# Optimization experiments

Hardware: AMD Instinct MI355X
Metric: run time of the kernel (lower is better)

## Reference

```python
import jax, jax.numpy as jnp
import numpy as np

N_NODES = 100000
N_EDGES = 1600000
D_IN = 64
D_OUT = 64
ALPHA = 0.5


def setup_inputs() -> dict:
    key = jax.random.key(0)
    k_x, k_ei, k_w, k_ws, k_bs, k_wd, k_bd = jax.random.split(key, 7)
    x = jax.random.normal(k_x, (N_NODES, D_IN), dtype=jnp.float32)
    edge_index = jax.random.randint(k_ei, (2, N_EDGES), 0, N_NODES, dtype=jnp.int64)
    edge_weight = jax.random.uniform(k_w, (N_EDGES,), dtype=jnp.float32)
    # torch Linear init: uniform(-1/sqrt(fan_in), 1/sqrt(fan_in))
    bound = 1.0 / np.sqrt(D_IN)
    W_src = jax.random.uniform(k_ws, (D_OUT, D_IN), minval=-bound, maxval=bound, dtype=jnp.float32)
    b_src = jax.random.uniform(k_bs, (D_OUT,), minval=-bound, maxval=bound, dtype=jnp.float32)
    W_dst = jax.random.uniform(k_wd, (D_OUT, D_IN), minval=-bound, maxval=bound, dtype=jnp.float32)
    b_dst = jax.random.uniform(k_bd, (D_OUT,), minval=-bound, maxval=bound, dtype=jnp.float32)
    return {"x": x, "edge_index": edge_index, "edge_weight": edge_weight,
            "W_src": W_src, "b_src": b_src, "W_dst": W_dst, "b_dst": b_dst}


def _dir_norm_spmm(row, col, w, x, n):
    """Compute (D_out^{-1/2} A D_in^{-1/2}) @ x for A with entries (row, col, w)."""
    out_deg = jax.ops.segment_sum(w, row, num_segments=n)  # row sums (dim=1)
    in_deg = jax.ops.segment_sum(w, col, num_segments=n)   # col sums (dim=0)
    d_out = jnp.where(out_deg > 0, out_deg ** -0.5, 0.0)
    d_in = jnp.where(in_deg > 0, in_deg ** -0.5, 0.0)
    w_norm = w * d_out[row] * d_in[col]                    # [E]
    # SpMM: out[i] = sum_{e: row_e = i} w_norm_e * x[col_e]
    return jax.ops.segment_sum(w_norm[:, None] * x[col], row, num_segments=n)


def reference(x, edge_index, edge_weight, W_src, b_src, W_dst, b_dst):
    row, col = edge_index[0], edge_index[1]
    n = x.shape[0]
    agg_fwd = _dir_norm_spmm(row, col, edge_weight, x, n)   # adj_norm @ x
    agg_bwd = _dir_norm_spmm(col, row, edge_weight, x, n)   # adj_t_norm @ x
    out = ALPHA * (agg_fwd @ W_src.T + b_src) + (1.0 - ALPHA) * (agg_bwd @ W_dst.T + b_dst)
    return out
```

## Files before the change

### kernel.cpp

```cpp
#include <hip/hip_runtime.h>

#define D 64
#define ALPHA 0.5f
#define FXSCALE 16777216.f
#define CE 2048
#define BSH 9
#define BN 512

typedef unsigned long long u64;
typedef unsigned short u16;
typedef unsigned int u32;
typedef float f32x4 __attribute__((ext_vector_type(4)));

static __device__ __forceinline__ u16 f2bf(float f) {
    unsigned u = __float_as_uint(f);
    unsigned r = (u + 0x7fffu + ((u >> 16) & 1u)) >> 16;
    return (u16)r;
}
static __device__ __forceinline__ float bf2f(u16 h) {
    return __uint_as_float(((unsigned)h) << 16);
}
static __device__ __forceinline__ float dinv_of_fx(u32 fx) {
    float s = (float)fx * (1.f / FXSCALE);
    return (s > 0.f) ? rsqrtf(s) : 0.f;
}

__global__ void p1_hist_kernel(const int* __restrict__ row, const int* __restrict__ col,
                               int* __restrict__ bh, int N, int E, int NCH, int NBUCK) {
    __shared__ u32 h[512];
    int t = threadIdx.x, ch = blockIdx.x;
    h[t] = 0;
    __syncthreads();
    int e0 = ch * CE, e1 = min(E, e0 + CE);
    for (int e = e0 + t; e < e1; e += 512) {
        atomicAdd(&h[(u32)row[e] >> BSH], 1u);
        atomicAdd(&h[(u32)(N + col[e]) >> BSH], 1u);
    }
    __syncthreads();
    for (int b = t; b < NBUCK; b += 512)
        bh[(size_t)b * NCH + ch] = (int)h[b];
}

__global__ void scan1i_kernel(const int* __restrict__ src, int* __restrict__ bsum, int SZ) {
    __shared__ int s[512];
    int t = threadIdx.x;
    int i = blockIdx.x * 512 + t;
    s[t] = (i < SZ) ? src[i] : 0;
    __syncthreads();
    for (int off = 256; off; off >>= 1) {
        if (t < off) s[t] += s[t + off];
        __syncthreads();
    }
    if (t == 0) bsum[blockIdx.x] = s[0];
}

__global__ void scan2w_kernel(int* __restrict__ bsum, int nb) {
    __shared__ int s[1024];
    int t = threadIdx.x;
    int v = (t < nb) ? bsum[t] : 0;
    s[t] = v;
    __syncthreads();
    for (int off = 1; off < 1024; off <<= 1) {
        int u = (t >= off) ? s[t - off] : 0;
        __syncthreads();
        s[t] += u;
        __syncthreads();
    }
    if (t < nb) bsum[t] = s[t] - v;
}

__global__ void scan3i_kernel(const int* __restrict__ src, const int* __restrict__ bsum,
                              int* __restrict__ dst, int SZ) {
    __shared__ int s[512];
    int t = threadIdx.x;
    int i = blockIdx.x * 512 + t;
    int v = (i < SZ) ? src[i] : 0;
    s[t] = v;
    __syncthreads();
    for (int off = 1; off < 512; off <<= 1) {
        int u = (t >= off) ? s[t - off] : 0;
        __syncthreads();
        s[t] += u;
        __syncthreads();
    }
    if (i < SZ) dst[i] = bsum[blockIdx.x] + s[t] - v;
}

__global__ void p3_sort_kernel(const int* __restrict__ row, const int* __restrict__ col,
                               const float* __restrict__ w,
                               const int* __restrict__ scanned,
                               u64* __restrict__ ent, int N, int E, int NCH, int NBUCK) {
    __shared__ u64 ebuf[4096];
    __shared__ u16 ebkt[4096];
    __shared__ u32 hc[512], hstart[512], hoff[512];
    __shared__ int s[512];
    int t = threadIdx.x, ch = blockIdx.x;
    hc[t] = 0;
    __syncthreads();
    int e0 = ch * CE, e1 = min(E, e0 + CE);
    for (int e = e0 + t; e < e1; e += 512) {
        atomicAdd(&hc[(u32)row[e] >> BSH], 1u);
        atomicAdd(&hc[(u32)(N + col[e]) >> BSH], 1u);
    }
    __syncthreads();
    int v = (int)hc[t];
    s[t] = v;
    __syncthreads();
    for (int off = 1; off < 512; off <<= 1) {
        int u = (t >= off) ? s[t - off] : 0;
        __syncthreads();
        s[t] += u;
        __syncthreads();
    }
    hstart[t] = (u32)(s[t] - v);
    hoff[t]   = (u32)(s[t] - v);
    hc[t] = (t < NBUCK) ? (u32)scanned[(size_t)t * NCH + ch] : 0u;
    __syncthreads();
    for (int e = e0 + t; e < e1; e += 512) {
        int r = row[e], c = col[e];
        u32 wb = __float_as_uint(w[e]);
        u32 b1 = (u32)r >> BSH;
        u64 q1 = ((u64)wb << 32) | ((u32)c << BSH) | ((u32)r & (BN - 1));
        u32 p1 = atomicAdd(&hoff[b1], 1u);
        ebuf[p1] = q1; ebkt[p1] = (u16)b1;
        u32 d2 = (u32)(N + c);
        u32 b2 = d2 >> BSH;
        u64 q2 = ((u64)wb << 32) | ((u32)r << BSH) | (d2 & (BN - 1));
        u32 p2 = atomicAdd(&hoff[b2], 1u);
        ebuf[p2] = q2; ebkt[p2] = (u16)b2;
    }
    __syncthreads();
    int nent = 2 * (e1 - e0);
    for (int p = t; p < nent; p += 512) {
        u32 b = ebkt[p];
        ent[(size_t)hc[b] + (u32)p - hstart[b]] = ebuf[p];
    }
}

__global__ void p4_build_kernel(const u64* __restrict__ ent, const int* __restrict__ scanned,
                                float* __restrict__ dinv, int* __restrict__ ptr,
                                float2* __restrict__ edata,
                                int L, int NCH, int NBUCK, int total) {
    __shared__ u32 cnt[512], fx[512], pstart[512], pfill[512];
    __shared__ int s[512];
    int t = threadIdx.x, b = blockIdx.x;
    int base0 = scanned[(size_t)b * NCH];
    int base1 = (b + 1 < NBUCK) ? scanned[(size_t)(b + 1) * NCH] : total;
    int nE = base1 - base0;
    cnt[t] = 0; fx[t] = 0;
    __syncthreads();
    for (int i = t; i < nE; i += 512) {
        u64 q = ent[base0 + i];
        u32 dlo = (u32)q & (BN - 1);
        float wv = __uint_as_float((u32)(q >> 32));
        atomicAdd(&cnt[dlo], 1u);
        atomicAdd(&fx[dlo], (u32)__float2uint_rn(wv * FXSCALE));
    }
    __syncthreads();
    int v = (int)cnt[t];
    s[t] = v;
    __syncthreads();
    for (int off = 1; off < 512; off <<= 1) {
        int u = (t >= off) ? s[t - off] : 0;
        __syncthreads();
        s[t] += u;
        __syncthreads();
    }
    pstart[t] = (u32)(s[t] - v);
    pfill[t]  = (u32)(s[t] - v);
    int node = b * BN + t;
    if (node < L) {
        dinv[node] = dinv_of_fx(fx[t]);
        ptr[node] = base0 + (int)pstart[t];
    }
    if (b == 0 && t == 0) ptr[L] = total;
    __syncthreads();
    for (int i = t; i < nE; i += 512) {
        u64 q = ent[base0 + i];
        u32 dlo = (u32)q & (BN - 1);
        u32 src = ((u32)q) >> BSH;
        float wv = __uint_as_float((u32)(q >> 32));
        u32 pos = atomicAdd(&pfill[dlo], 1u);
        edata[base0 + pos] = make_float2(__int_as_float((int)src), wv);
    }
}

__global__ void transform2r_kernel(const float* __restrict__ x,
                                   const float* __restrict__ Ws, const float* __restrict__ Wd,
                                   const float* __restrict__ dinv,
                                   u16* __restrict__ y1, u16* __restrict__ y2, int N) {
    __shared__ float xs[64][65];
    __shared__ float Wt1[64][68];
    __shared__ float Wt2[64][68];
    int t = threadIdx.x;
    for (int i = t; i < 4096; i += 256) {
        int o = i >> 6, k = i & 63;
        Wt1[k][o] = Ws[i];
        Wt2[k][o] = Wd[i];
    }
    int r0 = blockIdx.x * 64;
    for (int i = t; i < 4096; i += 256) {
        int r = i >> 6, k = i & 63;
        int gr = r0 + r;
        xs[r][k] = (gr < N) ? x[(size_t)gr * D + k] : 0.f;
    }
    __syncthreads();
    int ro = t >> 4, co = t & 15;
    float a1[4][4] = {}, a2[4][4] = {};
#pragma unroll 4
    for (int k = 0; k < 64; ++k) {
        float v0 = xs[ro * 4 + 0][k];
        float v1 = xs[ro * 4 + 1][k];
        float v2 = xs[ro * 4 + 2][k];
        float v3 = xs[ro * 4 + 3][k];
        float4 b1 = *(const float4*)&Wt1[k][co * 4];
        float4 b2 = *(const float4*)&Wt2[k][co * 4];
        a1[0][0] += v0 * b1.x; a1[0][1] += v0 * b1.y; a1[0][2] += v0 * b1.z; a1[0][3] += v0 * b1.w;
        a1[1][0] += v1 * b1.x; a1[1][1] += v1 * b1.y; a1[1][2] += v1 * b1.z; a1[1][3] += v1 * b1.w;
        a1[2][0] += v2 * b1.x; a1[2][1] += v2 * b1.y; a1[2][2] += v2 * b1.z; a1[2][3] += v2 * b1.w;
        a1[3][0] += v3 * b1.x; a1[3][1] += v3 * b1.y; a1[3][2] += v3 * b1.z; a1[3][3] += v3 * b1.w;
        a2[0][0] += v0 * b2.x; a2[0][1] += v0 * b2.y; a2[0][2] += v0 * b2.z; a2[0][3] += v0 * b2.w;
        a2[1][0] += v1 * b2.x; a2[1][1] += v1 * b2.y; a2[1][2] += v1 * b2.z; a2[1][3] += v1 * b2.w;
        a2[2][0] += v2 * b2.x; a2[2][1] += v2 * b2.y; a2[2][2] += v2 * b2.z; a2[2][3] += v2 * b2.w;
        a2[3][0] += v3 * b2.x; a2[3][1] += v3 * b2.y; a2[3][2] += v3 * b2.z; a2[3][3] += v3 * b2.w;
    }
#pragma unroll
    for (int i = 0; i < 4; ++i) {
        int gr = r0 + ro * 4 + i;
        if (gr < N) {
            float d1 = ALPHA * dinv[N + gr];
            float d2 = (1.f - ALPHA) * dinv[gr];
            ushort4 o1, o2;
            o1.x = f2bf(a1[i][0] * d1); o1.y = f2bf(a1[i][1] * d1);
            o1.z = f2bf(a1[i][2] * d1); o1.w = f2bf(a1[i][3] * d1);
            o2.x = f2bf(a2[i][0] * d2); o2.y = f2bf(a2[i][1] * d2);
            o2.z = f2bf(a2[i][2] * d2); o2.w = f2bf(a2[i][3] * d2);
            *(ushort4*)&y1[(size_t)gr * D + co * 4] = o1;
            *(ushort4*)&y2[(size_t)gr * D + co * 4] = o2;
        }
    }
}

__global__ void gather_csr_kernel(const int* __restrict__ ptr, const float* __restrict__ dinv,
                                  const float2* __restrict__ ed,
                                  const u16* __restrict__ y1, const u16* __restrict__ y2,
                                  const float* __restrict__ b_src, const float* __restrict__ b_dst,
                                  float* __restrict__ out, int N) {
    int tid = threadIdx.x;
    int lane = tid & 63;
    int node = blockIdx.x * (blockDim.x >> 6) + (tid >> 6);
    if (node >= N) return;
    int g  = lane >> 4;
    int fl = lane & 15;
    float dout = dinv[node], din = dinv[N + node];

    float f0 = 0.f, f1 = 0.f, f2 = 0.f, f3 = 0.f;
    float b0 = 0.f, b1 = 0.f, b2 = 0.f, b3 = 0.f;

    {
        int e0 = ptr[node], e1 = ptr[node + 1];
        for (int eb = e0; eb < e1; eb += 8) {
            int ea = eb + g, ex = eb + 4 + g;
            float2 da = (ea < e1) ? ed[ea] : make_float2(__int_as_float(0), 0.f);
            float2 db = (ex < e1) ? ed[ex] : make_float2(__int_as_float(0), 0.f);
            int sa = __float_as_int(da.x), sb = __float_as_int(db.x);
            float wa = da.y, wb = db.y;
            u64 qa = *(const u64*)(y1 + (((size_t)sa) << 6) + (fl << 2));
            u64 qb = *(const u64*)(y1 + (((size_t)sb) << 6) + (fl << 2));
            f0 += wa * bf2f((u16)qa)         + wb * bf2f((u16)qb);
            f1 += wa * bf2f((u16)(qa >> 16)) + wb * bf2f((u16)(qb >> 16));
            f2 += wa * bf2f((u16)(qa >> 32)) + wb * bf2f((u16)(qb >> 32));
            f3 += wa * bf2f((u16)(qa >> 48)) + wb * bf2f((u16)(qb >> 48));
        }
    }
    {
        int e0 = ptr[N + node], e1 = ptr[N + node + 1];
        for (int eb = e0; eb < e1; eb += 8) {
            int ea = eb + g, ex = eb + 4 + g;
            float2 da = (ea < e1) ? ed[ea] : make_float2(__int_as_float(0), 0.f);
            float2 db = (ex < e1) ? ed[ex] : make_float2(__int_as_float(0), 0.f);
            int sa = __float_as_int(da.x), sb = __float_as_int(db.x);
            float wa = da.y, wb = db.y;
            u64 qa = *(const u64*)(y2 + (((size_t)sa) << 6) + (fl << 2));
            u64 qb = *(const u64*)(y2 + (((size_t)sb) << 6) + (fl << 2));
            b0 += wa * bf2f((u16)qa)         + wb * bf2f((u16)qb);
            b1 += wa * bf2f((u16)(qa >> 16)) + wb * bf2f((u16)(qb >> 16));
            b2 += wa * bf2f((u16)(qa >> 32)) + wb * bf2f((u16)(qb >> 32));
            b3 += wa * bf2f((u16)(qa >> 48)) + wb * bf2f((u16)(qb >> 48));
        }
    }
    float v0 = f0 * dout + b0 * din;
    float v1 = f1 * dout + b1 * din;
    float v2 = f2 * dout + b2 * din;
    float v3 = f3 * dout + b3 * din;
    v0 += __shfl_xor(v0, 16); v0 += __shfl_xor(v0, 32);
    v1 += __shfl_xor(v1, 16); v1 += __shfl_xor(v1, 32);
    v2 += __shfl_xor(v2, 16); v2 += __shfl_xor(v2, 32);
    v3 += __shfl_xor(v3, 16); v3 += __shfl_xor(v3, 32);
    if (g == 0) {
        float4 bs = *(const float4*)&b_src[fl << 2];
        float4 bd = *(const float4*)&b_dst[fl << 2];
        f32x4 o;
        o.x = v0 + ALPHA * bs.x + (1.f - ALPHA) * bd.x;
        o.y = v1 + ALPHA * bs.y + (1.f - ALPHA) * bd.y;
        o.z = v2 + ALPHA * bs.z + (1.f - ALPHA) * bd.z;
        o.w = v3 + ALPHA * bs.w + (1.f - ALPHA) * bd.w;
        __builtin_nontemporal_store(o, (f32x4*)&out[((size_t)node << 6) + (fl << 2)]);
    }
}

extern "C" void kernel_launch(void* const* d_in, const int* in_sizes, int n_in,
                              void* d_out, int out_size, void* d_ws, size_t ws_size,
                              hipStream_t stream) {
    const float* x     = (const float*)d_in[0];
    const int*   ei    = (const int*)d_in[1];
    const float* w     = (const float*)d_in[2];
    const float* W_src = (const float*)d_in[3];
    const float* b_src = (const float*)d_in[4];
    const float* W_dst = (const float*)d_in[5];
    const float* b_dst = (const float*)d_in[6];
    float* out = (float*)d_out;

    const int N = in_sizes[0] / D;
    const int E = in_sizes[2];
    const int* row = ei;
    const int* col = ei + E;
    const int L = 2 * N;
    const int NCH   = (E + CE - 1) / CE;
    const int NBUCK = (L + BN - 1) >> BSH;
    const int SZ    = NBUCK * NCH;
    const int NSB   = (SZ + 511) / 512;
    const int total = 2 * E;

    char* base = (char*)d_ws;
    size_t o = 0;
    auto take = [&](size_t b) { char* p = base + o; o = (o + b + 63) & ~(size_t)63; return p; };
    int*    bh      = (int*)take((size_t)SZ * 4);
    int*    scanned = (int*)take((size_t)SZ * 4);
    int*    bsum    = (int*)take(1024 * 4);
    u64*    ent     = (u64*)take((size_t)total * 8);
    float*  dinv    = (float*)take((size_t)L * 4);
    int*    ptr     = (int*)take((size_t)(L + 1) * 4);
    u16*    y1      = (u16*)take((size_t)N * D * 2);
    u16*    y2      = (u16*)take((size_t)N * D * 2);
    float2* edata   = (float2*)take((size_t)total * 8);

    p1_hist_kernel<<<NCH, 512, 0, stream>>>(row, col, bh, N, E, NCH, NBUCK);
    scan1i_kernel<<<NSB, 512, 0, stream>>>(bh, bsum, SZ);
    scan2w_kernel<<<1, 1024, 0, stream>>>(bsum, NSB);
    scan3i_kernel<<<NSB, 512, 0, stream>>>(bh, bsum, scanned, SZ);
    p3_sort_kernel<<<NCH, 512, 0, stream>>>(row, col, w, scanned, ent, N, E, NCH, NBUCK);
    p4_build_kernel<<<NBUCK, 512, 0, stream>>>(ent, scanned, dinv, ptr, edata,
                                               L, NCH, NBUCK, total);
    transform2r_kernel<<<(N + 63) / 64, 256, 0, stream>>>(x, W_src, W_dst, dinv, y1, y2, N);
    gather_csr_kernel<<<(N + 3) / 4, 256, 0, stream>>>(ptr, dinv, edata, y1, y2,
                                                       b_src, b_dst, out, N);
}
```

Baseline: 233.7 us.

## Fuse dense transform into sort kernel and move source-degree scaling into gather

After: 217.1 us. 1.08x faster.

```diff
diff --git a/kernel.cpp b/kernel.cpp
--- a/kernel.cpp
+++ b/kernel.cpp
@@ -86,54 +86,111 @@
     if (i < SZ) dst[i] = bsum[blockIdx.x] + s[t] - v;
 }
 
-__global__ void p3_sort_kernel(const int* __restrict__ row, const int* __restrict__ col,
-                               const float* __restrict__ w,
-                               const int* __restrict__ scanned,
-                               u64* __restrict__ ent, int N, int E, int NCH, int NBUCK) {
-    __shared__ u64 ebuf[4096];
-    __shared__ u16 ebkt[4096];
-    __shared__ u32 hc[512], hstart[512], hoff[512];
-    __shared__ int s[512];
-    int t = threadIdx.x, ch = blockIdx.x;
-    hc[t] = 0;
-    __syncthreads();
-    int e0 = ch * CE, e1 = min(E, e0 + CE);
-    for (int e = e0 + t; e < e1; e += 512) {
-        atomicAdd(&hc[(u32)row[e] >> BSH], 1u);
-        atomicAdd(&hc[(u32)(N + col[e]) >> BSH], 1u);
-    }
-    __syncthreads();
-    int v = (int)hc[t];
-    s[t] = v;
-    __syncthreads();
-    for (int off = 1; off < 512; off <<= 1) {
-        int u = (t >= off) ? s[t - off] : 0;
-        __syncthreads();
-        s[t] += u;
-        __syncthreads();
-    }
-    hstart[t] = (u32)(s[t] - v);
-    hoff[t]   = (u32)(s[t] - v);
-    hc[t] = (t < NBUCK) ? (u32)scanned[(size_t)t * NCH + ch] : 0u;
-    __syncthreads();
-    for (int e = e0 + t; e < e1; e += 512) {
-        int r = row[e], c = col[e];
-        u32 wb = __float_as_uint(w[e]);
-        u32 b1 = (u32)r >> BSH;
-        u64 q1 = ((u64)wb << 32) | ((u32)c << BSH) | ((u32)r & (BN - 1));
-        u32 p1 = atomicAdd(&hoff[b1], 1u);
-        ebuf[p1] = q1; ebkt[p1] = (u16)b1;
-        u32 d2 = (u32)(N + c);
-        u32 b2 = d2 >> BSH;
-        u64 q2 = ((u64)wb << 32) | ((u32)r << BSH) | (d2 & (BN - 1));
-        u32 p2 = atomicAdd(&hoff[b2], 1u);
-        ebuf[p2] = q2; ebkt[p2] = (u16)b2;
-    }
-    __syncthreads();
-    int nent = 2 * (e1 - e0);
-    for (int p = t; p < nent; p += 512) {
-        u32 b = ebkt[p];
-        ent[(size_t)hc[b] + (u32)p - hstart[b]] = ebuf[p];
+__global__ __launch_bounds__(512)
+void p3_transform_kernel(const int* __restrict__ row, const int* __restrict__ col,
+                         const float* __restrict__ w, const int* __restrict__ scanned,
+                         u64* __restrict__ ent,
+                         const float* __restrict__ x,
+                         const float* __restrict__ Ws, const float* __restrict__ Wd,
+                         u16* __restrict__ y1, u16* __restrict__ y2,
+                         int N, int E, int NCH, int NBUCK, int NT, int total_blocks) {
+    __shared__ u64 smem[6432];
+    int b = blockIdx.x;
+    int t = threadIdx.x;
+    int t_before = (int)(((long long)b * NT) / total_blocks);
+    bool is_t = (int)(((long long)(b + 1) * NT) / total_blocks) > t_before;
+
+    if (!is_t) {
+        int ch = b - t_before;
+        u64* ebuf   = smem;
+        u16* ebkt   = (u16*)(smem + 4096);
+        u32* hc     = (u32*)(smem + 5120);
+        u32* hstart = (u32*)(smem + 5376);
+        u32* hoff   = (u32*)(smem + 5632);
+        int* s      = (int*)(smem + 5888);
+        hc[t] = 0;
+        __syncthreads();
+        int e0 = ch * CE, e1 = min(E, e0 + CE);
+        for (int e = e0 + t; e < e1; e += 512) {
+            atomicAdd(&hc[(u32)row[e] >> BSH], 1u);
+            atomicAdd(&hc[(u32)(N + col[e]) >> BSH], 1u);
+        }
+        __syncthreads();
+        int v = (int)hc[t];
+        s[t] = v;
+        __syncthreads();
+        for (int off = 1; off < 512; off <<= 1) {
+            int u = (t >= off) ? s[t - off] : 0;
+            __syncthreads();
+            s[t] += u;
+            __syncthreads();
+        }
+        hstart[t] = (u32)(s[t] - v);
+        hoff[t]   = (u32)(s[t] - v);
+        hc[t] = (t < NBUCK) ? (u32)scanned[(size_t)t * NCH + ch] : 0u;
+        __syncthreads();
+        for (int e = e0 + t; e < e1; e += 512) {
+            int r = row[e], c = col[e];
+            u32 wb = __float_as_uint(w[e]);
+            u32 b1 = (u32)r >> BSH;
+            u64 q1 = ((u64)wb << 32) | ((u32)c << BSH) | ((u32)r & (BN - 1));
+            u32 p1 = atomicAdd(&hoff[b1], 1u);
+            ebuf[p1] = q1; ebkt[p1] = (u16)b1;
+            u32 d2 = (u32)(N + c);
+            u32 b2 = d2 >> BSH;
+            u64 q2 = ((u64)wb << 32) | ((u32)r << BSH) | (d2 & (BN - 1));
+            u32 p2 = atomicAdd(&hoff[b2], 1u);
+            ebuf[p2] = q2; ebkt[p2] = (u16)b2;
+        }
+        __syncthreads();
+        int nent = 2 * (e1 - e0);
+        for (int p = t; p < nent; p += 512) {
+            u32 bb = ebkt[p];
+            ent[(size_t)hc[bb] + (u32)p - hstart[bb]] = ebuf[p];
+        }
+        return;
+    }
+
+    float* xs  = (float*)smem;
+    float* Wt1 = xs + 64 * 65;
+    float* Wt2 = Wt1 + 64 * 68;
+    for (int i = t; i < 4096; i += 512) {
+        int o = i >> 6, k = i & 63;
+        Wt1[k * 68 + o] = Ws[i];
+        Wt2[k * 68 + o] = Wd[i];
+    }
+    int r0 = t_before * 64;
+    for (int i = t; i < 4096; i += 512) {
+        int r = i >> 6, k = i & 63;
+        int gr = r0 + r;
+        xs[r * 65 + k] = (gr < N) ? x[(size_t)gr * D + k] : 0.f;
+    }
+    __syncthreads();
+    int ro = t >> 4, co = t & 15;
+    float a1[2][4] = {}, a2[2][4] = {};
+#pragma unroll 4
+    for (int k = 0; k < 64; ++k) {
+        float v0 = xs[(ro * 2 + 0) * 65 + k];
+        float v1 = xs[(ro * 2 + 1) * 65 + k];
+        float4 b1 = *(const float4*)&Wt1[k * 68 + co * 4];
+        float4 b2 = *(const float4*)&Wt2[k * 68 + co * 4];
+        a1[0][0] += v0 * b1.x; a1[0][1] += v0 * b1.y; a1[0][2] += v0 * b1.z; a1[0][3] += v0 * b1.w;
+        a1[1][0] += v1 * b1.x; a1[1][1] += v1 * b1.y; a1[1][2] += v1 * b1.z; a1[1][3] += v1 * b1.w;
+        a2[0][0] += v0 * b2.x; a2[0][1] += v0 * b2.y; a2[0][2] += v0 * b2.z; a2[0][3] += v0 * b2.w;
+        a2[1][0] += v1 * b2.x; a2[1][1] += v1 * b2.y; a2[1][2] += v1 * b2.z; a2[1][3] += v1 * b2.w;
+    }
+#pragma unroll
+    for (int i = 0; i < 2; ++i) {
+        int gr = r0 + ro * 2 + i;
+        if (gr < N) {
+            ushort4 o1, o2;
+            o1.x = f2bf(a1[i][0] * ALPHA); o1.y = f2bf(a1[i][1] * ALPHA);
+            o1.z = f2bf(a1[i][2] * ALPHA); o1.w = f2bf(a1[i][3] * ALPHA);
+            o2.x = f2bf(a2[i][0] * (1.f - ALPHA)); o2.y = f2bf(a2[i][1] * (1.f - ALPHA));
+            o2.z = f2bf(a2[i][2] * (1.f - ALPHA)); o2.w = f2bf(a2[i][3] * (1.f - ALPHA));
+            *(ushort4*)&y1[(size_t)gr * D + co * 4] = o1;
+            *(ushort4*)&y2[(size_t)gr * D + co * 4] = o2;
+        }
     }
 }
 
@@ -185,62 +242,6 @@
     }
 }
 
-__global__ void transform2r_kernel(const float* __restrict__ x,
-                                   const float* __restrict__ Ws, const float* __restrict__ Wd,
-                                   const float* __restrict__ dinv,
-                                   u16* __restrict__ y1, u16* __restrict__ y2, int N) {
-    __shared__ float xs[64][65];
-    __shared__ float Wt1[64][68];
-    __shared__ float Wt2[64][68];
-    int t = threadIdx.x;
-    for (int i = t; i < 4096; i += 256) {
-        int o = i >> 6, k = i & 63;
-        Wt1[k][o] = Ws[i];
-        Wt2[k][o] = Wd[i];
-    }
-    int r0 = blockIdx.x * 64;
-    for (int i = t; i < 4096; i += 256) {
-        int r = i >> 6, k = i & 63;
-        int gr = r0 + r;
-        xs[r][k] = (gr < N) ? x[(size_t)gr * D + k] : 0.f;
-    }
-    __syncthreads();
-    int ro = t >> 4, co = t & 15;
-    float a1[4][4] = {}, a2[4][4] = {};
-#pragma unroll 4
-    for (int k = 0; k < 64; ++k) {
-        float v0 = xs[ro * 4 + 0][k];
-        float v1 = xs[ro * 4 + 1][k];
-        float v2 = xs[ro * 4 + 2][k];
-        float v3 = xs[ro * 4 + 3][k];
-        float4 b1 = *(const float4*)&Wt1[k][co * 4];
-        float4 b2 = *(const float4*)&Wt2[k][co * 4];
-        a1[0][0] += v0 * b1.x; a1[0][1] += v0 * b1.y; a1[0][2] += v0 * b1.z; a1[0][3] += v0 * b1.w;
-        a1[1][0] += v1 * b1.x; a1[1][1] += v1 * b1.y; a1[1][2] += v1 * b1.z; a1[1][3] += v1 * b1.w;
-        a1[2][0] += v2 * b1.x; a1[2][1] += v2 * b1.y; a1[2][2] += v2 * b1.z; a1[2][3] += v2 * b1.w;
-        a1[3][0] += v3 * b1.x; a1[3][1] += v3 * b1.y; a1[3][2] += v3 * b1.z; a1[3][3] += v3 * b1.w;
-        a2[0][0] += v0 * b2.x; a2[0][1] += v0 * b2.y; a2[0][2] += v0 * b2.z; a2[0][3] += v0 * b2.w;
-        a2[1][0] += v1 * b2.x; a2[1][1] += v1 * b2.y; a2[1][2] += v1 * b2.z; a2[1][3] += v1 * b2.w;
-        a2[2][0] += v2 * b2.x; a2[2][1] += v2 * b2.y; a2[2][2] += v2 * b2.z; a2[2][3] += v2 * b2.w;
-        a2[3][0] += v3 * b2.x; a2[3][1] += v3 * b2.y; a2[3][2] += v3 * b2.z; a2[3][3] += v3 * b2.w;
-    }
-#pragma unroll
-    for (int i = 0; i < 4; ++i) {
-        int gr = r0 + ro * 4 + i;
-        if (gr < N) {
-            float d1 = ALPHA * dinv[N + gr];
-            float d2 = (1.f - ALPHA) * dinv[gr];
-            ushort4 o1, o2;
-            o1.x = f2bf(a1[i][0] * d1); o1.y = f2bf(a1[i][1] * d1);
-            o1.z = f2bf(a1[i][2] * d1); o1.w = f2bf(a1[i][3] * d1);
-            o2.x = f2bf(a2[i][0] * d2); o2.y = f2bf(a2[i][1] * d2);
-            o2.z = f2bf(a2[i][2] * d2); o2.w = f2bf(a2[i][3] * d2);
-            *(ushort4*)&y1[(size_t)gr * D + co * 4] = o1;
-            *(ushort4*)&y2[(size_t)gr * D + co * 4] = o2;
-        }
-    }
-}
-
 __global__ void gather_csr_kernel(const int* __restrict__ ptr, const float* __restrict__ dinv,
                                   const float2* __restrict__ ed,
                                   const u16* __restrict__ y1, const u16* __restrict__ y2,
@@ -252,47 +253,40 @@
     if (node >= N) return;
     int g  = lane >> 4;
     int fl = lane & 15;
-    float dout = dinv[node], din = dinv[N + node];
-
-    float f0 = 0.f, f1 = 0.f, f2 = 0.f, f3 = 0.f;
-    float b0 = 0.f, b1 = 0.f, b2 = 0.f, b3 = 0.f;
-
-    {
-        int e0 = ptr[node], e1 = ptr[node + 1];
-        for (int eb = e0; eb < e1; eb += 8) {
-            int ea = eb + g, ex = eb + 4 + g;
-            float2 da = (ea < e1) ? ed[ea] : make_float2(__int_as_float(0), 0.f);
-            float2 db = (ex < e1) ? ed[ex] : make_float2(__int_as_float(0), 0.f);
+
+    float v0 = 0.f, v1 = 0.f, v2 = 0.f, v3 = 0.f;
+#pragma unroll
+    for (int dir = 0; dir < 2; ++dir) {
+        const u16* __restrict__ y = dir ? y2 : y1;
+        const float* __restrict__ ds = dir ? dinv : dinv + N;
+        int e0 = ptr[dir * N + node], e1 = ptr[dir * N + node + 1];
+        float c0 = 0.f, c1 = 0.f, c2 = 0.f, c3 = 0.f;
+        for (int eb = e0; eb < e1; eb += 16) {
+            int ea = eb + g, eb2 = eb + 4 + g, ec = eb + 8 + g, ee = eb + 12 + g;
+            float2 da = (ea  < e1) ? ed[ea]  : make_float2(__int_as_float(0), 0.f);
+            float2 db = (eb2 < e1) ? ed[eb2] : make_float2(__int_as_float(0), 0.f);
+            float2 dc = (ec  < e1) ? ed[ec]  : make_float2(__int_as_float(0), 0.f);
+            float2 de = (ee  < e1) ? ed[ee]  : make_float2(__int_as_float(0), 0.f);
             int sa = __float_as_int(da.x), sb = __float_as_int(db.x);
-            float wa = da.y, wb = db.y;
-            u64 qa = *(const u64*)(y1 + (((size_t)sa) << 6) + (fl << 2));
-            u64 qb = *(const u64*)(y1 + (((size_t)sb) << 6) + (fl << 2));
-            f0 += wa * bf2f((u16)qa)         + wb * bf2f((u16)qb);
-            f1 += wa * bf2f((u16)(qa >> 16)) + wb * bf2f((u16)(qb >> 16));
-            f2 += wa * bf2f((u16)(qa >> 32)) + wb * bf2f((u16)(qb >> 32));
-            f3 += wa * bf2f((u16)(qa >> 48)) + wb * bf2f((u16)(qb >> 48));
-        }
-    }
-    {
-        int e0 = ptr[N + node], e1 = ptr[N + node + 1];
-        for (int eb = e0; eb < e1; eb += 8) {
-            int ea = eb + g, ex = eb + 4 + g;
-            float2 da = (ea < e1) ? ed[ea] : make_float2(__int_as_float(0), 0.f);
-            float2 db = (ex < e1) ? ed[ex] : make_float2(__int_as_float(0), 0.f);
-            int sa = __float_as_int(da.x), sb = __float_as_int(db.x);
-            float wa = da.y, wb = db.y;
-            u64 qa = *(const u64*)(y2 + (((size_t)sa) << 6) + (fl << 2));
-            u64 qb = *(const u64*)(y2 + (((size_t)sb) << 6) + (fl << 2));
-            b0 += wa * bf2f((u16)qa)         + wb * bf2f((u16)qb);
-            b1 += wa * bf2f((u16)(qa >> 16)) + wb * bf2f((u16)(qb >> 16));
-            b2 += wa * bf2f((u16)(qa >> 32)) + wb * bf2f((u16)(qb >> 32));
-            b3 += wa * bf2f((u16)(qa >> 48)) + wb * bf2f((u16)(qb >> 48));
-        }
-    }
-    float v0 = f0 * dout + b0 * din;
-    float v1 = f1 * dout + b1 * din;
-    float v2 = f2 * dout + b2 * din;
-    float v3 = f3 * dout + b3 * din;
+            int sc = __float_as_int(dc.x), se = __float_as_int(de.x);
+            float wa = da.y * ds[sa], wb = db.y * ds[sb];
+            float wc = dc.y * ds[sc], we = de.y * ds[se];
+            u64 qa = *(const u64*)(y + (((size_t)sa) << 6) + (fl << 2));
+            u64 qb = *(const u64*)(y + (((size_t)sb) << 6) + (fl << 2));
+            u64 qc = *(const u64*)(y + (((size_t)sc) << 6) + (fl << 2));
+            u64 qe = *(const u64*)(y + (((size_t)se) << 6) + (fl << 2));
+            c0 += wa * bf2f((u16)qa)         + wb * bf2f((u16)qb)
+                + wc * bf2f((u16)qc)         + we * bf2f((u16)qe);
+            c1 += wa * bf2f((u16)(qa >> 16)) + wb * bf2f((u16)(qb >> 16))
+                + wc * bf2f((u16)(qc >> 16)) + we * bf2f((u16)(qe >> 16));
+            c2 += wa * bf2f((u16)(qa >> 32)) + wb * bf2f((u16)(qb >> 32))
+                + wc * bf2f((u16)(qc >> 32)) + we * bf2f((u16)(qe >> 32));
+            c3 += wa * bf2f((u16)(qa >> 48)) + wb * bf2f((u16)(qb >> 48))
+                + wc * bf2f((u16)(qc >> 48)) + we * bf2f((u16)(qe >> 48));
+        }
+        float scale = dinv[dir * N + node];
+        v0 += c0 * scale; v1 += c1 * scale; v2 += c2 * scale; v3 += c3 * scale;
+    }
     v0 += __shfl_xor(v0, 16); v0 += __shfl_xor(v0, 32);
     v1 += __shfl_xor(v1, 16); v1 += __shfl_xor(v1, 32);
     v2 += __shfl_xor(v2, 16); v2 += __shfl_xor(v2, 32);
@@ -330,6 +324,7 @@
     const int NBUCK = (L + BN - 1) >> BSH;
     const int SZ    = NBUCK * NCH;
     const int NSB   = (SZ + 511) / 512;
+    const int NT    = (N + 63) / 64;
     const int total = 2 * E;
 
     char* base = (char*)d_ws;
@@ -349,10 +344,11 @@
     scan1i_kernel<<<NSB, 512, 0, stream>>>(bh, bsum, SZ);
     scan2w_kernel<<<1, 1024, 0, stream>>>(bsum, NSB);
     scan3i_kernel<<<NSB, 512, 0, stream>>>(bh, bsum, scanned, SZ);
-    p3_sort_kernel<<<NCH, 512, 0, stream>>>(row, col, w, scanned, ent, N, E, NCH, NBUCK);
+    p3_transform_kernel<<<NCH + NT, 512, 0, stream>>>(row, col, w, scanned, ent,
+                                                      x, W_src, W_dst, y1, y2,
+                                                      N, E, NCH, NBUCK, NT, NCH + NT);
     p4_build_kernel<<<NBUCK, 512, 0, stream>>>(ent, scanned, dinv, ptr, edata,
                                                L, NCH, NBUCK, total);
-    transform2r_kernel<<<(N + 63) / 64, 256, 0, stream>>>(x, W_src, W_dst, dinv, y1, y2, N);
     gather_csr_kernel<<<(N + 3) / 4, 256, 0, stream>>>(ptr, dinv, edata, y1, y2,
                                                        b_src, b_dst, out, N);
 }
```
